# Optimization experiments

Measured on AMD Instinct MI355X. Metric: run time of the kernel, lower is better.

## Reference

```python
import jax, jax.numpy as jnp
import numpy as np

N = 100000
E_HALF = 800000
DIM = 128
NB, BD = 8, 4
HID = 256  # dim * hidden_dim_multiplier
TIME = 21
NUM_ATT = 5


def setup_inputs() -> dict:
    key = jax.random.key(0)
    ks = jax.random.split(key, 8)
    x = jax.random.normal(ks[0], (N, DIM), jnp.float32)
    node_rep = jax.random.normal(ks[1], (N, NB, BD, BD), jnp.float32)
    s = jax.random.randint(ks[2], (E_HALF,), 0, N)
    d = jax.random.randint(ks[3], (E_HALF,), 0, N)
    src = jnp.concatenate([s, d])  # symmetric graph -> every endpoint has out_degree >= 1
    dst = jnp.concatenate([d, s])
    attention = jax.random.uniform(ks[4], (NUM_ATT,), jnp.float32)
    W1 = jax.random.normal(ks[5], (DIM, HID), jnp.float32) / np.sqrt(DIM)
    b1 = jnp.zeros((HID,), jnp.float32)
    W2 = jax.random.normal(ks[6], (HID, DIM), jnp.float32) / np.sqrt(HID)
    b2 = jnp.zeros((DIM,), jnp.float32)
    return {"x": x, "node_rep": node_rep, "src": src, "dst": dst,
            "attention": attention, "W1": W1, "b1": b1, "W2": W2, "b2": b2}


def reference(x, node_rep, src, dst, attention, W1, b1, W2, b2):
    n, dim = x.shape
    nb, bd = node_rep.shape[1], node_rep.shape[2]
    # out_degrees and symmetric-norm coefficients per edge (u_mul_v then 1/sqrt)
    deg = jax.ops.segment_sum(jnp.ones(src.shape, x.dtype), src, num_segments=n)
    norm = 1.0 / jnp.sqrt(deg[src] * deg[dst])  # [E]

    # bundle transform: einsum('abcd,abde->abce', node_rep, x.reshape(n,nb,bd,-1))
    vf = x.reshape(n, nb, bd, -1)
    vf = jnp.einsum('abcd,abde->abce', node_rep, vf)
    h = vf.reshape(n, dim)

    def prop(h):  # u_mul_e_sum: sum over in-edges of h[src] * norm[edge]
        msg = h[src] * norm[:, None]           # [E, dim]
        return jax.ops.segment_sum(msg, dst, num_segments=n)

    snap_idx = {1: 0, 2: 1, 5: 2, 20: 3}
    diff = jnp.zeros((NUM_ATT, n, dim), x.dtype)  # slot 4 never written in source; zeroed
    for t in range(1, TIME + 1):
        h = prop(h)
        if t in snap_idx:
            diff = diff.at[snap_idx[t]].set(h)

    att = jax.nn.softmax(attention)
    h = jnp.einsum('a,acb->cb', att, diff)  # [n, dim]

    # feed-forward (dropout=0; torch GELU default = exact erf)
    h = jax.nn.gelu(h @ W1 + b1, approximate=False)
    h = h @ W2 + b2

    # inverse bundle transform with node_rep transposed on last two dims
    vf = h.reshape(n, nb, bd, -1)
    vf = jnp.einsum('abcd,abde->abce', jnp.swapaxes(node_rep, 2, 3), vf)
    message = vf.reshape(n, dim)
    return jnp.concatenate([x, message], axis=1)  # [n, 2*dim]
```

## Files before the change

### kernel.cpp

```cpp
#include <hip/hip_runtime.h>
#include <hip/hip_fp16.h>
#include <math.h>

#define DIM 128
#define HID 256

typedef _Float16 f16;
typedef f16 f16x8 __attribute__((ext_vector_type(8)));
typedef float f32x4 __attribute__((ext_vector_type(4)));
typedef float f32x2 __attribute__((ext_vector_type(2)));

__device__ __forceinline__ float gelu_exact(float x) {
    return 0.5f * x * (1.0f + erff(x * 0.70710678118654752f));
}
__device__ __forceinline__ float2 h2f2(unsigned u) {
    __half2 h;
    *reinterpret_cast<unsigned*>(&h) = u;
    return __half22float2(h);
}
__device__ __forceinline__ unsigned f2h2(float a, float b) {
    __half2 h = __floats2half2_rn(a, b);
    return *reinterpret_cast<unsigned*>(&h);
}
__device__ __forceinline__ unsigned fp8pk4(float a, float b, float c, float d) {
    unsigned r = (unsigned)__builtin_amdgcn_cvt_pk_fp8_f32(a, b, 0, false);
    r = (unsigned)__builtin_amdgcn_cvt_pk_fp8_f32(c, d, (int)r, true);
    return r;
}

__global__ __launch_bounds__(256) void k_deg(const int* __restrict__ src, int* __restrict__ deg, int E) {
    int e = blockIdx.x * 256 + threadIdx.x;
    if (e < E) atomicAdd(&deg[src[e]], 1);
}

__global__ __launch_bounds__(256) void k_dscale(const int* __restrict__ deg, float* __restrict__ invdeg,
                                                float* __restrict__ sqdeg, int n) {
    int v = blockIdx.x * 256 + threadIdx.x;
    if (v >= n) return;
    float d = (float)deg[v];
    invdeg[v] = 1.0f / d;
    sqdeg[v] = sqrtf(d);
}

__global__ __launch_bounds__(256) void k_scan_part(const int* __restrict__ deg, int* __restrict__ bsum, int n) {
    __shared__ int sred[256];
    int base = blockIdx.x * 1024 + threadIdx.x * 4;
    int s = 0;
#pragma unroll
    for (int k = 0; k < 4; ++k) { int i = base + k; if (i < n) s += deg[i]; }
    sred[threadIdx.x] = s; __syncthreads();
    for (int st = 128; st > 0; st >>= 1) {
        if (threadIdx.x < st) sred[threadIdx.x] += sred[threadIdx.x + st];
        __syncthreads();
    }
    if (threadIdx.x == 0) bsum[blockIdx.x] = sred[0];
}

__global__ void k_scan_bsum(int* bsum, int nb, int* offs, int n, int E) {
    if (threadIdx.x == 0 && blockIdx.x == 0) {
        int run = 0;
        for (int b = 0; b < nb; ++b) { int t = bsum[b]; bsum[b] = run; run += t; }
        offs[n] = E;
    }
}

__global__ __launch_bounds__(256) void k_scan_off(const int* __restrict__ deg, const int* __restrict__ bsum,
                                                  int* __restrict__ offs, int n) {
    __shared__ int sps[256];
    int tid = threadIdx.x;
    int base = blockIdx.x * 1024 + tid * 4;
    int v[4]; int s = 0;
#pragma unroll
    for (int k = 0; k < 4; ++k) { int i = base + k; v[k] = (i < n) ? deg[i] : 0; s += v[k]; }
    sps[tid] = s; __syncthreads();
    for (int st = 1; st < 256; st <<= 1) {
        int add = (tid >= st) ? sps[tid - st] : 0;
        __syncthreads();
        sps[tid] += add;
        __syncthreads();
    }
    int run = sps[tid] - s + bsum[blockIdx.x];
#pragma unroll
    for (int k = 0; k < 4; ++k) { int i = base + k; if (i < n) offs[i] = run; run += v[k]; }
}

__global__ __launch_bounds__(256) void k_fill(const int* __restrict__ src, const int* __restrict__ dst,
                                              const int* __restrict__ offs, int* __restrict__ cursor,
                                              unsigned* __restrict__ cedge, int E) {
    int e = blockIdx.x * 256 + threadIdx.x;
    if (e >= E) return;
    int s = src[e], d = dst[e];
    int pos = offs[d] + atomicAdd(&cursor[d], 1);
    cedge[pos] = (unsigned)s;
}

__global__ __launch_bounds__(256) void k_bundle(const float* __restrict__ x, const float* __restrict__ nr,
                                                const int* __restrict__ deg, unsigned char* __restrict__ h, int n) {
    int t = blockIdx.x * 256 + threadIdx.x;
    if (t >= n * 8) return;
    int node = t >> 3, b = t & 7;
    float rs = rsqrtf((float)deg[node]);
    const float4* Xp = (const float4*)(x + (size_t)node * DIM + b * 16);
    const float4* Rp = (const float4*)(nr + (size_t)node * DIM + b * 16);
    float4 X[4], R[4];
#pragma unroll
    for (int k = 0; k < 4; ++k) { X[k] = Xp[k]; R[k] = Rp[k]; }
    unsigned o[4];
#pragma unroll
    for (int c = 0; c < 4; ++c) {
        float4 Rc = R[c];
        float4 O;
        O.x = fmaf(Rc.x, X[0].x, fmaf(Rc.y, X[1].x, fmaf(Rc.z, X[2].x, Rc.w * X[3].x)));
        O.y = fmaf(Rc.x, X[0].y, fmaf(Rc.y, X[1].y, fmaf(Rc.z, X[2].y, Rc.w * X[3].y)));
        O.z = fmaf(Rc.x, X[0].z, fmaf(Rc.y, X[1].z, fmaf(Rc.z, X[2].z, Rc.w * X[3].z)));
        O.w = fmaf(Rc.x, X[0].w, fmaf(Rc.y, X[1].w, fmaf(Rc.z, X[2].w, Rc.w * X[3].w)));
        o[c] = fp8pk4(O.x * rs, O.y * rs, O.z * rs, O.w * rs);
    }
    *(uint4*)(h + (size_t)node * DIM + b * 16) = make_uint4(o[0], o[1], o[2], o[3]);
}

__global__ void k_softmax(const float* __restrict__ a, float* __restrict__ att) {
    if (threadIdx.x != 0 || blockIdx.x != 0) return;
    float m = a[0];
    for (int i = 1; i < 5; ++i) m = fmaxf(m, a[i]);
    float e[5], ssum = 0.f;
    for (int i = 0; i < 5; ++i) { e[i] = expf(a[i] - m); ssum += e[i]; }
    for (int i = 0; i < 5; ++i) att[i] = e[i] / ssum;
}

__global__ __launch_bounds__(256) void k_wcvt(const float* __restrict__ W1, const float* __restrict__ W2,
                                              f16* __restrict__ W1T, f16* __restrict__ W2T) {
    int t = blockIdx.x * 256 + threadIdx.x;
    if (t < DIM * HID) {
        int k = t >> 8, j = t & 255;
        W1T[(size_t)j * DIM + k] = (f16)W1[(size_t)k * HID + j];
        int j2 = t >> 7, i = t & 127;
        W2T[(size_t)i * HID + j2] = (f16)W2[(size_t)j2 * DIM + i];
    }
}

__device__ __forceinline__ void acc8f8(float* f, uint2 h) {
    f32x2 p0 = __builtin_amdgcn_cvt_pk_f32_fp8(h.x, false);
    f32x2 p1 = __builtin_amdgcn_cvt_pk_f32_fp8(h.x, true);
    f32x2 p2 = __builtin_amdgcn_cvt_pk_f32_fp8(h.y, false);
    f32x2 p3 = __builtin_amdgcn_cvt_pk_f32_fp8(h.y, true);
    f[0] += p0.x; f[1] += p0.y; f[2] += p1.x; f[3] += p1.y;
    f[4] += p2.x; f[5] += p2.y; f[6] += p3.x; f[7] += p3.y;
}

__global__ __launch_bounds__(256, 8) void k_prop(const uint2* __restrict__ hin, uint2* __restrict__ hout,
                                                 const int* __restrict__ offs, const unsigned* __restrict__ cedge,
                                                 const float* __restrict__ invdeg, int n) {
    int v = blockIdx.x * 16 + (threadIdx.x >> 4);
    if (v >= n) return;
    int lane = threadIdx.x & 15;
    int b = offs[v], e = offs[v + 1];
    float f[8], g[8];
#pragma unroll
    for (int k = 0; k < 8; ++k) { f[k] = 0.f; g[k] = 0.f; }
    const uint2* hb = hin + lane;
    int m4 = (e - b) >> 2;
    int i = b;
    if (m4 > 0) {
        unsigned e0 = cedge[i], e1 = cedge[i + 1], e2 = cedge[i + 2], e3 = cedge[i + 3];
        for (int t = 0; t < m4; ++t) {
            uint2 h0 = hb[(size_t)e0 * 16];
            uint2 h1 = hb[(size_t)e1 * 16];
            uint2 h2 = hb[(size_t)e2 * 16];
            uint2 h3 = hb[(size_t)e3 * 16];
            i += 4;
            if (t + 1 < m4) {
                e0 = cedge[i]; e1 = cedge[i + 1]; e2 = cedge[i + 2]; e3 = cedge[i + 3];
            }
            acc8f8(f, h0); acc8f8(g, h1); acc8f8(f, h2); acc8f8(g, h3);
        }
    }
    for (; i < e; ++i) {
        uint2 h0 = hb[(size_t)cedge[i] * 16];
        acc8f8(f, h0);
    }
    float idv = invdeg[v];
    uint2 ov;
    ov.x = fp8pk4((f[0] + g[0]) * idv, (f[1] + g[1]) * idv, (f[2] + g[2]) * idv, (f[3] + g[3]) * idv);
    ov.y = fp8pk4((f[4] + g[4]) * idv, (f[5] + g[5]) * idv, (f[6] + g[6]) * idv, (f[7] + g[7]) * idv);
    hout[(size_t)v * 16 + lane] = ov;
}

#define SA_LD 136
#define SH_LD 264
__global__ __launch_bounds__(256, 3) void k_ffn_mfma(const unsigned char* __restrict__ S0,
                                                     const unsigned char* __restrict__ S1,
                                                     const unsigned char* __restrict__ S2,
                                                     const unsigned char* __restrict__ S3,
                                                     const float* __restrict__ attv, const float* __restrict__ sqdeg,
                                                     const f16* __restrict__ W1T, const float* __restrict__ b1,
                                                     const f16* __restrict__ W2T, const float* __restrict__ b2,
                                                     __half* __restrict__ outb, int n) {
    __shared__ f16 sA[64 * SA_LD];
    __shared__ f16 sH[64 * SH_LD];
    int tid = threadIdx.x;
    int wid = tid >> 6;
    int lane = tid & 63;
    int row16 = lane & 15;
    int kgrp = lane >> 4;
    int r0 = blockIdx.x * 64;
    float a0 = attv[0], a1 = attv[1], a2 = attv[2], a3 = attv[3];

    const uint2* p0 = (const uint2*)S0;
    const uint2* p1 = (const uint2*)S1;
    const uint2* p2 = (const uint2*)S2;
    const uint2* p3 = (const uint2*)S3;
    for (int idx = tid; idx < 64 * 16; idx += 256) {
        int r = idx >> 4;
        int ch = idx & 15;
        int row = r0 + r; row = (row < n) ? row : (n - 1);
        float sd = sqdeg[row];
        float w0 = a0 * sd, w1 = a1 * sd, w2 = a2 * sd, w3 = a3 * sd;
        size_t u = (size_t)row * 16 + ch;
        uint2 x0 = p0[u], x1 = p1[u], x2 = p2[u], x3 = p3[u];
        float rv[8];
#pragma unroll
        for (int half = 0; half < 2; ++half) {
            unsigned q0 = half ? x0.y : x0.x, q1 = half ? x1.y : x1.x;
            unsigned q2 = half ? x2.y : x2.x, q3 = half ? x3.y : x3.x;
            f32x2 d0l = __builtin_amdgcn_cvt_pk_f32_fp8(q0, false);
            f32x2 d0h = __builtin_amdgcn_cvt_pk_f32_fp8(q0, true);
            f32x2 d1l = __builtin_amdgcn_cvt_pk_f32_fp8(q1, false);
            f32x2 d1h = __builtin_amdgcn_cvt_pk_f32_fp8(q1, true);
            f32x2 d2l = __builtin_amdgcn_cvt_pk_f32_fp8(q2, false);
            f32x2 d2h = __builtin_amdgcn_cvt_pk_f32_fp8(q2, true);
            f32x2 d3l = __builtin_amdgcn_cvt_pk_f32_fp8(q3, false);
            f32x2 d3h = __builtin_amdgcn_cvt_pk_f32_fp8(q3, true);
            rv[half * 4 + 0] = w0 * d0l.x + w1 * d1l.x + w2 * d2l.x + w3 * d3l.x;
            rv[half * 4 + 1] = w0 * d0l.y + w1 * d1l.y + w2 * d2l.y + w3 * d3l.y;
            rv[half * 4 + 2] = w0 * d0h.x + w1 * d1h.x + w2 * d2h.x + w3 * d3h.x;
            rv[half * 4 + 3] = w0 * d0h.y + w1 * d1h.y + w2 * d2h.y + w3 * d3h.y;
        }
        *(uint4*)(&sA[r * SA_LD + ch * 8]) = make_uint4(f2h2(rv[0], rv[1]), f2h2(rv[2], rv[3]),
                                                        f2h2(rv[4], rv[5]), f2h2(rv[6], rv[7]));
    }
    __syncthreads();

    {
        float bias1[4];
#pragma unroll
        for (int nt = 0; nt < 4; ++nt) bias1[nt] = b1[wid * 64 + nt * 16 + row16];
        f32x4 c1[4][4];
#pragma unroll
        for (int mt = 0; mt < 4; ++mt)
#pragma unroll
            for (int nt = 0; nt < 4; ++nt) c1[mt][nt] = (f32x4){0.f, 0.f, 0.f, 0.f};
        for (int ks = 0; ks < 4; ++ks) {
            f16x8 a[4], b[4];
#pragma unroll
            for (int mt = 0; mt < 4; ++mt)
                a[mt] = *(const f16x8*)(&sA[(mt * 16 + row16) * SA_LD + ks * 32 + kgrp * 8]);
#pragma unroll
            for (int nt = 0; nt < 4; ++nt)
                b[nt] = *(const f16x8*)(W1T + (size_t)(wid * 64 + nt * 16 + row16) * DIM + ks * 32 + kgrp * 8);
#pragma unroll
            for (int mt = 0; mt < 4; ++mt)
#pragma unroll
                for (int nt = 0; nt < 4; ++nt)
                    c1[mt][nt] = __builtin_amdgcn_mfma_f32_16x16x32_f16(a[mt], b[nt], c1[mt][nt], 0, 0, 0);
        }
#pragma unroll
        for (int mt = 0; mt < 4; ++mt)
#pragma unroll
            for (int nt = 0; nt < 4; ++nt) {
                int srow = mt * 16 + kgrp * 4;
                int scol = wid * 64 + nt * 16 + row16;
#pragma unroll
                for (int r = 0; r < 4; ++r) {
                    float v = c1[mt][nt][r] + bias1[nt];
                    sH[(srow + r) * SH_LD + scol] = (f16)gelu_exact(v);
                }
            }
    }
    __syncthreads();

    {
        float bias2[2];
#pragma unroll
        for (int nt = 0; nt < 2; ++nt) bias2[nt] = b2[wid * 32 + nt * 16 + row16];
        f32x4 c2[4][2];
#pragma unroll
        for (int mt = 0; mt < 4; ++mt)
#pragma unroll
            for (int nt = 0; nt < 2; ++nt) c2[mt][nt] = (f32x4){0.f, 0.f, 0.f, 0.f};
        for (int ks = 0; ks < 8; ++ks) {
            f16x8 a[4], b[2];
#pragma unroll
            for (int mt = 0; mt < 4; ++mt)
                a[mt] = *(const f16x8*)(&sH[(mt * 16 + row16) * SH_LD + ks * 32 + kgrp * 8]);
#pragma unroll
            for (int nt = 0; nt < 2; ++nt)
                b[nt] = *(const f16x8*)(W2T + (size_t)(wid * 32 + nt * 16 + row16) * HID + ks * 32 + kgrp * 8);
#pragma unroll
            for (int mt = 0; mt < 4; ++mt)
#pragma unroll
                for (int nt = 0; nt < 2; ++nt)
                    c2[mt][nt] = __builtin_amdgcn_mfma_f32_16x16x32_f16(a[mt], b[nt], c2[mt][nt], 0, 0, 0);
        }
#pragma unroll
        for (int mt = 0; mt < 4; ++mt)
#pragma unroll
            for (int nt = 0; nt < 2; ++nt) {
                int col = wid * 32 + nt * 16 + row16;
#pragma unroll
                for (int r = 0; r < 4; ++r) {
                    int row = r0 + mt * 16 + kgrp * 4 + r;
                    if (row < n) outb[(size_t)row * DIM + col] = (__half)(c2[mt][nt][r] + bias2[nt]);
                }
            }
    }
}

__global__ __launch_bounds__(256) void k_inv_out(const float* __restrict__ x, const float* __restrict__ nr,
                                                 const __half* __restrict__ hf, float* __restrict__ out, int n) {
    int t = blockIdx.x * 256 + threadIdx.x;
    if (t >= n * 8) return;
    int node = t >> 3, b = t & 7;
    const float4* Xin = (const float4*)(x + (size_t)node * DIM + b * 16);
    float4* Ox = (float4*)(out + (size_t)node * 2 * DIM + b * 16);
#pragma unroll
    for (int k = 0; k < 4; ++k) Ox[k] = Xin[k];
    const uint4* Hp = (const uint4*)(hf + (size_t)node * DIM + b * 16);
    uint4 hlo = Hp[0], hhi = Hp[1];
    float4 H[4];
    {
        float2 u0 = h2f2(hlo.x), u1 = h2f2(hlo.y);
        H[0] = make_float4(u0.x, u0.y, u1.x, u1.y);
        float2 u2 = h2f2(hlo.z), u3 = h2f2(hlo.w);
        H[1] = make_float4(u2.x, u2.y, u3.x, u3.y);
        float2 u4 = h2f2(hhi.x), u5 = h2f2(hhi.y);
        H[2] = make_float4(u4.x, u4.y, u5.x, u5.y);
        float2 u6 = h2f2(hhi.z), u7 = h2f2(hhi.w);
        H[3] = make_float4(u6.x, u6.y, u7.x, u7.y);
    }
    const float4* Rp = (const float4*)(nr + (size_t)node * DIM + b * 16);
    float4 R[4];
#pragma unroll
    for (int k = 0; k < 4; ++k) R[k] = Rp[k];
    float4* Om = (float4*)(out + (size_t)node * 2 * DIM + DIM + b * 16);
    {
        float4 O;
        O.x = fmaf(R[0].x, H[0].x, fmaf(R[1].x, H[1].x, fmaf(R[2].x, H[2].x, R[3].x * H[3].x)));
        O.y = fmaf(R[0].x, H[0].y, fmaf(R[1].x, H[1].y, fmaf(R[2].x, H[2].y, R[3].x * H[3].y)));
        O.z = fmaf(R[0].x, H[0].z, fmaf(R[1].x, H[1].z, fmaf(R[2].x, H[2].z, R[3].x * H[3].z)));
        O.w = fmaf(R[0].x, H[0].w, fmaf(R[1].x, H[1].w, fmaf(R[2].x, H[2].w, R[3].x * H[3].w)));
        Om[0] = O;
    }
    {
        float4 O;
        O.x = fmaf(R[0].y, H[0].x, fmaf(R[1].y, H[1].x, fmaf(R[2].y, H[2].x, R[3].y * H[3].x)));
        O.y = fmaf(R[0].y, H[0].y, fmaf(R[1].y, H[1].y, fmaf(R[2].y, H[2].y, R[3].y * H[3].y)));
        O.z = fmaf(R[0].y, H[0].z, fmaf(R[1].y, H[1].z, fmaf(R[2].y, H[2].z, R[3].y * H[3].z)));
        O.w = fmaf(R[0].y, H[0].w, fmaf(R[1].y, H[1].w, fmaf(R[2].y, H[2].w, R[3].y * H[3].w)));
        Om[1] = O;
    }
    {
        float4 O;
        O.x = fmaf(R[0].z, H[0].x, fmaf(R[1].z, H[1].x, fmaf(R[2].z, H[2].x, R[3].z * H[3].x)));
        O.y = fmaf(R[0].z, H[0].y, fmaf(R[1].z, H[1].y, fmaf(R[2].z, H[2].y, R[3].z * H[3].y)));
        O.z = fmaf(R[0].z, H[0].z, fmaf(R[1].z, H[1].z, fmaf(R[2].z, H[2].z, R[3].z * H[3].z)));
        O.w = fmaf(R[0].z, H[0].w, fmaf(R[1].z, H[1].w, fmaf(R[2].z, H[2].w, R[3].z * H[3].w)));
        Om[2] = O;
    }
    {
        float4 O;
        O.x = fmaf(R[0].w, H[0].x, fmaf(R[1].w, H[1].x, fmaf(R[2].w, H[2].x, R[3].w * H[3].x)));
        O.y = fmaf(R[0].w, H[0].y, fmaf(R[1].w, H[1].y, fmaf(R[2].w, H[2].y, R[3].w * H[3].y)));
        O.z = fmaf(R[0].w, H[0].z, fmaf(R[1].w, H[1].z, fmaf(R[2].w, H[2].z, R[3].w * H[3].z)));
        O.w = fmaf(R[0].w, H[0].w, fmaf(R[1].w, H[1].w, fmaf(R[2].w, H[2].w, R[3].w * H[3].w)));
        Om[3] = O;
    }
}

extern "C" void kernel_launch(void* const* d_in, const int* in_sizes, int n_in,
                              void* d_out, int out_size, void* d_ws, size_t ws_size,
                              hipStream_t stream) {
    const float* x         = (const float*)d_in[0];
    const float* nrep      = (const float*)d_in[1];
    const int*   src       = (const int*)d_in[2];
    const int*   dst       = (const int*)d_in[3];
    const float* attention = (const float*)d_in[4];
    const float* W1        = (const float*)d_in[5];
    const float* b1        = (const float*)d_in[6];
    const float* W2        = (const float*)d_in[7];
    const float* b2        = (const float*)d_in[8];
    float* out = (float*)d_out;

    int n = in_sizes[0] / DIM;
    int E = in_sizes[2];

    char* w = (char*)d_ws;
    size_t off = 0;
    auto alloc = [&](size_t bytes) -> char* {
        char* p = w + off;
        off = (off + bytes + 255) & ~(size_t)255;
        return p;
    };
    size_t hbytes = (size_t)n * DIM;
    int*      deg    = (int*)alloc((size_t)n * 4);
    int*      cursor = (int*)alloc((size_t)n * 4);
    int*      offs   = (int*)alloc((size_t)(n + 1) * 4);
    int       nb     = (n + 1023) / 1024;
    int*      bsum   = (int*)alloc((size_t)nb * 4);
    float*    attbuf = (float*)alloc(8 * 4);
    float*    invdeg = (float*)alloc((size_t)n * 4);
    float*    sqdeg  = (float*)alloc((size_t)n * 4);
    unsigned* cedge  = (unsigned*)alloc((size_t)E * 4);
    char*     region = alloc(hbytes * 2);
    unsigned char* B0 = (unsigned char*)region;
    unsigned char* T1 = (unsigned char*)(region + hbytes);
    __half*   ffin   = (__half*)region;
    unsigned char* S[4];
    for (int k = 0; k < 4; ++k) S[k] = (unsigned char*)alloc(hbytes);
    f16*      W1T    = (f16*)alloc((size_t)DIM * HID * 2);
    f16*      W2T    = (f16*)alloc((size_t)DIM * HID * 2);

    hipMemsetAsync(deg, 0, (size_t)n * 4, stream);
    hipMemsetAsync(cursor, 0, (size_t)n * 4, stream);

    k_deg<<<(E + 255) / 256, 256, 0, stream>>>(src, deg, E);
    k_dscale<<<(n + 255) / 256, 256, 0, stream>>>(deg, invdeg, sqdeg, n);
    k_scan_part<<<nb, 256, 0, stream>>>(deg, bsum, n);
    k_scan_bsum<<<1, 64, 0, stream>>>(bsum, nb, offs, n, E);
    k_scan_off<<<nb, 256, 0, stream>>>(deg, bsum, offs, n);
    k_fill<<<(E + 255) / 256, 256, 0, stream>>>(src, dst, offs, cursor, cedge, E);
    k_bundle<<<(n * 8 + 255) / 256, 256, 0, stream>>>(x, nrep, deg, B0, n);
    k_softmax<<<1, 64, 0, stream>>>(attention, attbuf);
    k_wcvt<<<(DIM * HID + 255) / 256, 256, 0, stream>>>(W1, W2, W1T, W2T);

    unsigned char* cur = B0;
    for (int t = 1; t <= 20; ++t) {
        int snap = (t == 1) ? 0 : (t == 2) ? 1 : (t == 5) ? 2 : (t == 20) ? 3 : -1;
        unsigned char* nxt = (snap >= 0) ? S[snap] : ((cur == B0) ? T1 : B0);
        k_prop<<<(n + 15) / 16, 256, 0, stream>>>((const uint2*)cur, (uint2*)nxt, offs, cedge, invdeg, n);
        cur = nxt;
    }
    k_ffn_mfma<<<(n + 63) / 64, 256, 0, stream>>>(S[0], S[1], S[2], S[3], attbuf, sqdeg,
                                                  W1T, b1, W2T, b2, ffin, n);
    k_inv_out<<<(n * 8 + 255) / 256, 256, 0, stream>>>(x, nrep, ffin, out, n);
}
```

Before: 914.9 us.

## Tile CSR adjacency by source range so propagation gathers stay L2-resident

Edges are bucketed by (source tile of 16384 nodes, destination) into a two-level CSR, and degrees are derived from the tiled offsets. The propagation kernel becomes a fixed grid of 1024 blocks in which each 16-lane group owns up to 7 destination nodes. It walks the source tiles in order, keeping per-node accumulators in registers, so the gathered fp8 feature rows for one tile can stay in L2 across many destinations. The cost is more registers and lower occupancy, shorter inner loops with less memory-level parallelism, and a larger scan over n*NT entries. The fixed grid only covers n up to 1024*16*7 nodes.

```diff
diff --git a/kernel.cpp b/kernel.cpp
--- a/kernel.cpp
+++ b/kernel.cpp
@@ -4,6 +4,8 @@
 
 #define DIM 128
 #define HID 256
+#define TSHIFT 14
+#define KMAX 7
 
 typedef _Float16 f16;
 typedef f16 f16x8 __attribute__((ext_vector_type(8)));
@@ -28,18 +30,25 @@
     return r;
 }
 
-__global__ __launch_bounds__(256) void k_deg(const int* __restrict__ src, int* __restrict__ deg, int E) {
+__global__ __launch_bounds__(256) void k_deg2(const int* __restrict__ src, const int* __restrict__ dst,
+                                              int* __restrict__ deg2, int E, int n) {
     int e = blockIdx.x * 256 + threadIdx.x;
-    if (e < E) atomicAdd(&deg[src[e]], 1);
-}
-
-__global__ __launch_bounds__(256) void k_dscale(const int* __restrict__ deg, float* __restrict__ invdeg,
-                                                float* __restrict__ sqdeg, int n) {
+    if (e >= E) return;
+    int s = src[e], d = dst[e];
+    atomicAdd(&deg2[(s >> TSHIFT) * n + d], 1);
+}
+
+__global__ __launch_bounds__(256) void k_dscale(const int* __restrict__ offs2, float* __restrict__ invdeg,
+                                                float* __restrict__ sqdeg, float* __restrict__ rsq,
+                                                int n, int nt) {
     int v = blockIdx.x * 256 + threadIdx.x;
     if (v >= n) return;
-    float d = (float)deg[v];
+    int deg = 0;
+    for (int t = 0; t < nt; ++t) deg += offs2[t * n + v + 1] - offs2[t * n + v];
+    float d = (float)deg;
     invdeg[v] = 1.0f / d;
     sqdeg[v] = sqrtf(d);
+    rsq[v] = rsqrtf(d);
 }
 
 __global__ __launch_bounds__(256) void k_scan_part(const int* __restrict__ deg, int* __restrict__ bsum, int n) {
@@ -85,21 +94,22 @@
 }
 
 __global__ __launch_bounds__(256) void k_fill(const int* __restrict__ src, const int* __restrict__ dst,
-                                              const int* __restrict__ offs, int* __restrict__ cursor,
-                                              unsigned* __restrict__ cedge, int E) {
+                                              const int* __restrict__ offs2, int* __restrict__ cursor2,
+                                              unsigned* __restrict__ cedge, int E, int n) {
     int e = blockIdx.x * 256 + threadIdx.x;
     if (e >= E) return;
     int s = src[e], d = dst[e];
-    int pos = offs[d] + atomicAdd(&cursor[d], 1);
+    int idx = (s >> TSHIFT) * n + d;
+    int pos = offs2[idx] + atomicAdd(&cursor2[idx], 1);
     cedge[pos] = (unsigned)s;
 }
 
 __global__ __launch_bounds__(256) void k_bundle(const float* __restrict__ x, const float* __restrict__ nr,
-                                                const int* __restrict__ deg, unsigned char* __restrict__ h, int n) {
+                                                const float* __restrict__ rsq, unsigned char* __restrict__ h, int n) {
     int t = blockIdx.x * 256 + threadIdx.x;
     if (t >= n * 8) return;
     int node = t >> 3, b = t & 7;
-    float rs = rsqrtf((float)deg[node]);
+    float rs = rsq[node];
     const float4* Xp = (const float4*)(x + (size_t)node * DIM + b * 16);
     const float4* Rp = (const float4*)(nr + (size_t)node * DIM + b * 16);
     float4 X[4], R[4];
@@ -148,42 +158,52 @@
     f[4] += p2.x; f[5] += p2.y; f[6] += p3.x; f[7] += p3.y;
 }
 
-__global__ __launch_bounds__(256, 8) void k_prop(const uint2* __restrict__ hin, uint2* __restrict__ hout,
-                                                 const int* __restrict__ offs, const unsigned* __restrict__ cedge,
-                                                 const float* __restrict__ invdeg, int n) {
-    int v = blockIdx.x * 16 + (threadIdx.x >> 4);
-    if (v >= n) return;
+__global__ __launch_bounds__(256, 4) void k_prop(const uint2* __restrict__ hin, uint2* __restrict__ hout,
+                                                 const int* __restrict__ offs2, const unsigned* __restrict__ cedge,
+                                                 const float* __restrict__ invdeg, int n, int nt) {
+    int slot = blockIdx.x * 16 + (threadIdx.x >> 4);
     int lane = threadIdx.x & 15;
-    int b = offs[v], e = offs[v + 1];
-    float f[8], g[8];
-#pragma unroll
-    for (int k = 0; k < 8; ++k) { f[k] = 0.f; g[k] = 0.f; }
+    int nslots = gridDim.x * 16;
     const uint2* hb = hin + lane;
-    int m4 = (e - b) >> 2;
-    int i = b;
-    if (m4 > 0) {
-        unsigned e0 = cedge[i], e1 = cedge[i + 1], e2 = cedge[i + 2], e3 = cedge[i + 3];
-        for (int t = 0; t < m4; ++t) {
-            uint2 h0 = hb[(size_t)e0 * 16];
-            uint2 h1 = hb[(size_t)e1 * 16];
-            uint2 h2 = hb[(size_t)e2 * 16];
-            uint2 h3 = hb[(size_t)e3 * 16];
-            i += 4;
-            if (t + 1 < m4) {
-                e0 = cedge[i]; e1 = cedge[i + 1]; e2 = cedge[i + 2]; e3 = cedge[i + 3];
+    float acc[KMAX][8];
+#pragma unroll
+    for (int k = 0; k < KMAX; ++k)
+#pragma unroll
+        for (int j = 0; j < 8; ++j) acc[k][j] = 0.f;
+
+    for (int t = 0; t < nt; ++t) {
+        const int* ob = offs2 + (size_t)t * n;
+#pragma unroll
+        for (int k = 0; k < KMAX; ++k) {
+            int v = slot + k * nslots;
+            if (v < n) {
+                int b = ob[v], e = ob[v + 1];
+                int i = b;
+                for (; i + 2 <= e; i += 2) {
+                    unsigned e0 = cedge[i], e1 = cedge[i + 1];
+                    uint2 h0 = hb[(size_t)e0 * 16];
+                    uint2 h1 = hb[(size_t)e1 * 16];
+                    acc8f8(acc[k], h0);
+                    acc8f8(acc[k], h1);
+                }
+                if (i < e) {
+                    uint2 h0 = hb[(size_t)cedge[i] * 16];
+                    acc8f8(acc[k], h0);
+                }
             }
-            acc8f8(f, h0); acc8f8(g, h1); acc8f8(f, h2); acc8f8(g, h3);
         }
     }
-    for (; i < e; ++i) {
-        uint2 h0 = hb[(size_t)cedge[i] * 16];
-        acc8f8(f, h0);
-    }
-    float idv = invdeg[v];
-    uint2 ov;
-    ov.x = fp8pk4((f[0] + g[0]) * idv, (f[1] + g[1]) * idv, (f[2] + g[2]) * idv, (f[3] + g[3]) * idv);
-    ov.y = fp8pk4((f[4] + g[4]) * idv, (f[5] + g[5]) * idv, (f[6] + g[6]) * idv, (f[7] + g[7]) * idv);
-    hout[(size_t)v * 16 + lane] = ov;
+#pragma unroll
+    for (int k = 0; k < KMAX; ++k) {
+        int v = slot + k * nslots;
+        if (v < n) {
+            float idv = invdeg[v];
+            uint2 ov;
+            ov.x = fp8pk4(acc[k][0] * idv, acc[k][1] * idv, acc[k][2] * idv, acc[k][3] * idv);
+            ov.y = fp8pk4(acc[k][4] * idv, acc[k][5] * idv, acc[k][6] * idv, acc[k][7] * idv);
+            hout[(size_t)v * 16 + lane] = ov;
+        }
+    }
 }
 
 #define SA_LD 136
@@ -393,6 +413,8 @@
 
     int n = in_sizes[0] / DIM;
     int E = in_sizes[2];
+    int NT = (n + (1 << TSHIFT) - 1) >> TSHIFT;
+    int n2 = n * NT;
 
     char* w = (char*)d_ws;
     size_t off = 0;
@@ -402,34 +424,35 @@
         return p;
     };
     size_t hbytes = (size_t)n * DIM;
-    int*      deg    = (int*)alloc((size_t)n * 4);
-    int*      cursor = (int*)alloc((size_t)n * 4);
-    int*      offs   = (int*)alloc((size_t)(n + 1) * 4);
-    int       nb     = (n + 1023) / 1024;
-    int*      bsum   = (int*)alloc((size_t)nb * 4);
-    float*    attbuf = (float*)alloc(8 * 4);
-    float*    invdeg = (float*)alloc((size_t)n * 4);
-    float*    sqdeg  = (float*)alloc((size_t)n * 4);
-    unsigned* cedge  = (unsigned*)alloc((size_t)E * 4);
-    char*     region = alloc(hbytes * 2);
+    int*      deg2    = (int*)alloc((size_t)n2 * 4);
+    int*      cursor2 = (int*)alloc((size_t)n2 * 4);
+    int*      offs2   = (int*)alloc((size_t)(n2 + 1) * 4);
+    int       nb2     = (n2 + 1023) / 1024;
+    int*      bsum    = (int*)alloc((size_t)nb2 * 4);
+    float*    attbuf  = (float*)alloc(8 * 4);
+    float*    invdeg  = (float*)alloc((size_t)n * 4);
+    float*    sqdeg   = (float*)alloc((size_t)n * 4);
+    float*    rsq     = (float*)alloc((size_t)n * 4);
+    unsigned* cedge   = (unsigned*)alloc((size_t)E * 4);
+    char*     region  = alloc(hbytes * 2);
     unsigned char* B0 = (unsigned char*)region;
     unsigned char* T1 = (unsigned char*)(region + hbytes);
-    __half*   ffin   = (__half*)region;
+    __half*   ffin    = (__half*)region;
     unsigned char* S[4];
     for (int k = 0; k < 4; ++k) S[k] = (unsigned char*)alloc(hbytes);
-    f16*      W1T    = (f16*)alloc((size_t)DIM * HID * 2);
-    f16*      W2T    = (f16*)alloc((size_t)DIM * HID * 2);
-
-    hipMemsetAsync(deg, 0, (size_t)n * 4, stream);
-    hipMemsetAsync(cursor, 0, (size_t)n * 4, stream);
-
-    k_deg<<<(E + 255) / 256, 256, 0, stream>>>(src, deg, E);
-    k_dscale<<<(n + 255) / 256, 256, 0, stream>>>(deg, invdeg, sqdeg, n);
-    k_scan_part<<<nb, 256, 0, stream>>>(deg, bsum, n);
-    k_scan_bsum<<<1, 64, 0, stream>>>(bsum, nb, offs, n, E);
-    k_scan_off<<<nb, 256, 0, stream>>>(deg, bsum, offs, n);
-    k_fill<<<(E + 255) / 256, 256, 0, stream>>>(src, dst, offs, cursor, cedge, E);
-    k_bundle<<<(n * 8 + 255) / 256, 256, 0, stream>>>(x, nrep, deg, B0, n);
+    f16*      W1T     = (f16*)alloc((size_t)DIM * HID * 2);
+    f16*      W2T     = (f16*)alloc((size_t)DIM * HID * 2);
+
+    hipMemsetAsync(deg2, 0, (size_t)n2 * 4, stream);
+    hipMemsetAsync(cursor2, 0, (size_t)n2 * 4, stream);
+
+    k_deg2<<<(E + 255) / 256, 256, 0, stream>>>(src, dst, deg2, E, n);
+    k_scan_part<<<nb2, 256, 0, stream>>>(deg2, bsum, n2);
+    k_scan_bsum<<<1, 64, 0, stream>>>(bsum, nb2, offs2, n2, E);
+    k_scan_off<<<nb2, 256, 0, stream>>>(deg2, bsum, offs2, n2);
+    k_dscale<<<(n + 255) / 256, 256, 0, stream>>>(offs2, invdeg, sqdeg, rsq, n, NT);
+    k_fill<<<(E + 255) / 256, 256, 0, stream>>>(src, dst, offs2, cursor2, cedge, E, n);
+    k_bundle<<<(n * 8 + 255) / 256, 256, 0, stream>>>(x, nrep, rsq, B0, n);
     k_softmax<<<1, 64, 0, stream>>>(attention, attbuf);
     k_wcvt<<<(DIM * HID + 255) / 256, 256, 0, stream>>>(W1, W2, W1T, W2T);
 
@@ -437,7 +460,7 @@
     for (int t = 1; t <= 20; ++t) {
         int snap = (t == 1) ? 0 : (t == 2) ? 1 : (t == 5) ? 2 : (t == 20) ? 3 : -1;
         unsigned char* nxt = (snap >= 0) ? S[snap] : ((cur == B0) ? T1 : B0);
-        k_prop<<<(n + 15) / 16, 256, 0, stream>>>((const uint2*)cur, (uint2*)nxt, offs, cedge, invdeg, n);
+        k_prop<<<1024, 256, 0, stream>>>((const uint2*)cur, (uint2*)nxt, offs2, cedge, invdeg, n, NT);
         cur = nxt;
     }
     k_ffn_mfma<<<(n + 63) / 64, 256, 0, stream>>>(S[0], S[1], S[2], S[3], attbuf, sqdeg,
```

Measured after the change: 2.230 ms. 144% more time.
